# Optimization experiments

Measured on AMD Instinct MI355X. Metric: run time of the kernel, lower is better.

Reference implementation:

```python
import jax, jax.numpy as jnp
import numpy as np

NPOINT, RADIUS, NSAMPLE = 1024, 0.2, 32
EPS = 1e-5


def _fps(xyz, npoint):
    # Iterative farthest point sampling (deterministic start at index 0).
    B, N, _ = xyz.shape
    def step(carry, _):
        distance, farthest = carry
        centroid = jnp.take_along_axis(xyz, farthest[:, None, None], axis=1)  # (B,1,3)
        d = jnp.sum((xyz - centroid) ** 2, -1)                                # (B,N)
        distance = jnp.minimum(distance, d)
        return (distance, jnp.argmax(distance, -1)), farthest
    init = (jnp.full((B, N), 1e10, xyz.dtype), jnp.zeros((B,), jnp.int32))
    _, idx = jax.lax.scan(step, init, None, length=npoint)
    return idx.T  # (B, npoint)


def _gather(points, idx):
    # points (B,N,C), idx (B,S,K) -> (B,S,K,C)
    B, S, K = idx.shape
    flat = jnp.take_along_axis(points, idx.reshape(B, S * K)[:, :, None], axis=1)
    return flat.reshape(B, S, K, points.shape[-1])


def _query_ball(xyz, new_xyz):
    # For each centroid, first NSAMPLE point indices within RADIUS (pad with first hit).
    B, N, _ = xyz.shape
    sqr = jnp.sum((new_xyz[:, :, None, :] - xyz[:, None, :, :]) ** 2, -1)  # (B,S,N)
    gi = jnp.where(sqr > RADIUS ** 2, N, jnp.arange(N, dtype=jnp.int32)[None, None, :])
    gi = jnp.sort(gi, axis=-1)[:, :, :NSAMPLE]
    return jnp.where(gi == N, gi[:, :, :1], gi)  # (B,S,K)


def _cond_layer(x, t_embed, wt, bt, wc, bc, g, b):
    # ConditionalConv1d: x += time_mlp(gelu(t)); 1x1 conv; BatchNorm (batch stats); GELU.
    tp = jax.nn.gelu(t_embed, approximate=False) @ wt.T + bt      # (B,Cin)
    x = x + tp[:, None, None, :]
    y = jnp.einsum('bskc,oc->bsko', x, wc) + bc                   # (B,S,K,Cout)
    mu = jnp.mean(y, axis=(0, 1, 2))
    var = jnp.var(y, axis=(0, 1, 2))
    y = (y - mu) * jax.lax.rsqrt(var + EPS) * g + b
    return jax.nn.gelu(y, approximate=False)


def _forward(xyz, points, t_embed, params):
    fps_idx = _fps(xyz, NPOINT)                                        # (B,S)
    new_xyz = jnp.take_along_axis(xyz, fps_idx[:, :, None], axis=1)    # (B,S,3)
    idx = _query_ball(xyz, new_xyz)                                    # (B,S,K)
    grouped_xyz = _gather(xyz, idx) - new_xyz[:, :, None, :]           # (B,S,K,3)
    grouped_pts = _gather(jnp.swapaxes(points, 1, 2), idx)             # (B,S,K,C)
    x = jnp.concatenate([grouped_xyz, grouped_pts], -1)                # (B,S,K,C+3)
    for p in params:
        x = _cond_layer(x, t_embed, *p)
    new_points = jnp.swapaxes(jnp.max(x, axis=2), 1, 2)                # (B,Cout,S)
    return new_xyz, new_points


def setup_inputs() -> dict:
    key = jax.random.key(0)
    ks = iter(jax.random.split(key, 32))
    B, N, CIN, T = 8, 4096, 64, 128
    chans = [(CIN + 3, 64), (64, 64), (64, 128)]
    inp = {
        "xyz": jax.random.normal(next(ks), (B, N, 3), jnp.float32),
        "points": jax.random.normal(next(ks), (B, CIN, N), jnp.float32),
        "t_embed": jax.random.normal(next(ks), (B, T), jnp.float32),
    }
    for i, (ci, co) in enumerate(chans):
        inp[f"wt{i}"] = jax.random.normal(next(ks), (ci, T), jnp.float32) * 0.05
        inp[f"bt{i}"] = jnp.zeros((ci,), jnp.float32)
        inp[f"wc{i}"] = jax.random.normal(next(ks), (co, ci), jnp.float32) * 0.1
        inp[f"bc{i}"] = jnp.zeros((co,), jnp.float32)
        inp[f"g{i}"] = jnp.ones((co,), jnp.float32)
        inp[f"be{i}"] = jnp.zeros((co,), jnp.float32)
    return inp


def reference(xyz, points, t_embed,
              wt0, bt0, wc0, bc0, g0, be0,
              wt1, bt1, wc1, bc1, g1, be1,
              wt2, bt2, wc2, bc2, g2, be2):
    params = [(wt0, bt0, wc0, bc0, g0, be0),
              (wt1, bt1, wc1, bc1, g1, be1),
              (wt2, bt2, wc2, bc2, g2, be2)]
    return _forward(xyz, points, t_embed, params)
```

## Files before the change

kernel.cpp:

```cpp
#include <hip/hip_runtime.h>
#include <cmath>

#define Bc 8
#define Nc 4096
#define Sc 1024
#define Kc 32
#define Mc (Bc*Sc*Kc)

typedef float v2f __attribute__((ext_vector_type(2)));

__device__ __forceinline__ float gelu_f(float x){
  return 0.5f*x*(1.0f + erff(x*0.70710678f));
}

__device__ __forceinline__ v2f pk_add(v2f a, v2f b){
  v2f d; asm("v_pk_add_f32 %0, %1, %2" : "=v"(d) : "v"(a), "v"(b)); return d;
}
__device__ __forceinline__ v2f pk_mul(v2f a, v2f b){
  v2f d; asm("v_pk_mul_f32 %0, %1, %2" : "=v"(d) : "v"(a), "v"(b)); return d;
}

#define ROR_MAXF(v, n) { int _t = __builtin_amdgcn_update_dpp(__float_as_int(v), __float_as_int(v), 0x120|(n), 0xF, 0xF, false); \
                         v = fmaxf(v, __int_as_float(_t)); }
#define BC15_MAXF(v)   { int _t = __builtin_amdgcn_update_dpp(__float_as_int(v), __float_as_int(v), 0x142, 0xA, 0xF, false); \
                         v = fmaxf(v, __int_as_float(_t)); }
#define BC31_MAXF(v)   { int _t = __builtin_amdgcn_update_dpp(__float_as_int(v), __float_as_int(v), 0x143, 0xC, 0xF, false); \
                         v = fmaxf(v, __int_as_float(_t)); }

#define TK(v_, i_) { const bool _t = ((v_) > Bv) || (((v_) == Bv) && ((i_) < Bi)); \
  Bv = _t ? (v_) : Bv; Bi = _t ? (i_) : Bi; }

__global__ __launch_bounds__(256) void fused_front_kernel(
    const float* __restrict__ xyz, float* __restrict__ new_xyz,
    const float* __restrict__ points, float* __restrict__ pointsT,
    const float* __restrict__ t_embed,
    const float* __restrict__ wt0, const float* __restrict__ bt0,
    const float* __restrict__ wt1, const float* __restrict__ bt1,
    const float* __restrict__ wt2, const float* __restrict__ bt2,
    float* __restrict__ tp)
{
  __shared__ __align__(16) float smem[17424];
  const int bid = blockIdx.x;
  const int tid = threadIdx.x;

  if (bid < 8){
    const int b = bid;
    const int lane = tid & 63;
    const int wv = tid >> 6;
    const float* xb = xyz + b*Nc*3;
    float*    skv   = smem;
    unsigned* ski   = (unsigned*)(smem + 8);
    int*      shist = (int*)(smem + 16);
    float4*   c4    = (float4*)(smem + 1040);

    const int base = tid << 4;
    float4 f[12];
    const float4* src = (const float4*)(xb + base*3);
#pragma unroll
    for (int q=0;q<12;++q) f[q] = src[q];
#define AR(i) ((i)%4==0 ? f[(i)/4].x : (i)%4==1 ? f[(i)/4].y : (i)%4==2 ? f[(i)/4].z : f[(i)/4].w)
    v2f px2[8], py2[8], pz2[8], d2[8];
#pragma unroll
    for (int k=0;k<8;++k){
      px2[k].x = AR(6*k+0); py2[k].x = AR(6*k+1); pz2[k].x = AR(6*k+2);
      px2[k].y = AR(6*k+3); py2[k].y = AR(6*k+4); pz2[k].y = AR(6*k+5);
      c4[base+2*k  ] = make_float4(px2[k].x, py2[k].x, pz2[k].x, 0.f);
      c4[base+2*k+1] = make_float4(px2[k].y, py2[k].y, pz2[k].y, 0.f);
      d2[k].x = 1e10f; d2[k].y = 1e10f;
    }
#undef AR
    __syncthreads();
    int widx = 0;
    for (int it=0; it<Sc; ++it){
      const float4 cc = c4[widx];
      if (tid==0) shist[it] = widx;
      v2f ncx, ncy, ncz;
      ncx.x=-cc.x; ncx.y=-cc.x; ncy.x=-cc.y; ncy.y=-cc.y; ncz.x=-cc.z; ncz.y=-cc.z;
      float bvx=-1.0f, bvy=-1.0f;
#pragma unroll
      for (int k=0;k<8;++k){
        const v2f dx = pk_add(px2[k], ncx);
        const v2f dy = pk_add(py2[k], ncy);
        const v2f dz = pk_add(pz2[k], ncz);
        const v2f dd = pk_add(pk_add(pk_mul(dx,dx), pk_mul(dy,dy)), pk_mul(dz,dz));
        v2f dn;
        dn.x = fminf(d2[k].x, dd.x);
        dn.y = fminf(d2[k].y, dd.y);
        d2[k] = dn;
        bvx = fmaxf(bvx, dn.x);
        bvy = fmaxf(bvy, dn.y);
      }
      const float bv = fmaxf(bvx, bvy);
      unsigned bi_local = 0xFFFFFFFFu;
#pragma unroll
      for (int k=0;k<8;++k){
        const unsigned c0 = (d2[k].x == bv) ? (unsigned)(base + 2*k    ) : 0xFFFFFFFFu;
        const unsigned c1 = (d2[k].y == bv) ? (unsigned)(base + 2*k + 1) : 0xFFFFFFFFu;
        const unsigned cm = (c0 < c1) ? c0 : c1;
        bi_local = (cm < bi_local) ? cm : bi_local;
      }
      float mv = bv;
      ROR_MAXF(mv,1); ROR_MAXF(mv,2); ROR_MAXF(mv,4); ROR_MAXF(mv,8);
      BC15_MAXF(mv); BC31_MAXF(mv);
      mv = __int_as_float(__builtin_amdgcn_readlane(__float_as_int(mv), 63));
      const unsigned long long mk = __ballot(bv == mv);
      const int src_lane = __ffsll(mk) - 1;
      const unsigned bi = (unsigned)__builtin_amdgcn_readlane((int)bi_local, src_lane);
      const int p4 = (it & 1) << 2;
      if (lane==0){ skv[p4+wv] = mv; ski[p4+wv] = bi; }
      __syncthreads();
      const float4 m4 = *reinterpret_cast<const float4*>(&skv[p4]);
      const uint4  i4 = *reinterpret_cast<const uint4*>(&ski[p4]);
      float Bv = m4.x; unsigned Bi = i4.x;
      TK(m4.y, i4.y) TK(m4.z, i4.z) TK(m4.w, i4.w)
      widx = (int)Bi;
    }
    __syncthreads();
    for (int i = tid; i < Sc; i += 256){
      const float4 cc = c4[shist[i]];
      float* o = new_xyz + ((size_t)b*Sc + i)*3;
      o[0]=cc.x; o[1]=cc.y; o[2]=cc.z;
    }
  } else if (bid < 520){
    const int t  = bid - 8;
    const int tb = t >> 6;
    const int n0 = (t & 63) << 6;
    float (*tile)[65] = (float(*)[65])smem;
    const int sub = tid >> 6;
    const int ln  = tid & 63;
#pragma unroll 4
    for (int cp=0; cp<16; ++cp){
      const int c = (cp<<2) + sub;
      tile[c][ln] = points[((size_t)(tb*64+c))*Nc + n0 + ln];
    }
    __syncthreads();
#pragma unroll 4
    for (int np=0; np<16; ++np){
      const int nl = (np<<2) + sub;
      pointsT[((size_t)(tb*Nc + n0 + nl))*64 + ln] = tile[ln][nl];
    }
  } else {
    float* ge = smem;
    for (int i = tid; i < Bc*128; i += 256) ge[i] = gelu_f(t_embed[i]);
    __syncthreads();
    for (int i = tid; i < 3*Bc*68; i += 256){
      const int l = i / (Bc*68);
      const int r = i - l*(Bc*68);
      const int b = r / 68;
      const int c = r - b*68;
      const int ci = (l==0) ? 67 : 64;
      float v = 0.0f;
      if (c < ci){
        const float* wt = (l==0)?wt0:((l==1)?wt1:wt2);
        const float* bt = (l==0)?bt0:((l==1)?bt1:bt2);
        const float* w = wt + c*128;
        const float* g = ge + b*128;
        float acc = 0.0f;
        for (int t2=0;t2<128;++t2) acc = fmaf(g[t2], w[t2], acc);
        v = acc + bt[c];
      }
      tp[i] = v;
    }
  }
}

__global__ __launch_bounds__(256) void ballgather_kernel(const float* __restrict__ xyz,
    const float* __restrict__ new_xyz, const float* __restrict__ pointsT,
    float* __restrict__ X){
  const int g = (blockIdx.x<<2) + (threadIdx.x>>6);
  const int lane = threadIdx.x & 63;
  const int w = threadIdx.x >> 6;
  const int b = g >> 10;
  const float* xb = xyz + b*Nc*3;
  const float cx = new_xyz[g*3+0];
  const float cy = new_xyz[g*3+1];
  const float cz = new_xyz[g*3+2];
  __shared__ int sidx[4][32];
  int total = 0;
  for (int base=0; base<Nc; base+=64){
    const int i = base + lane;
    float dx=__fsub_rn(cx, xb[i*3+0]);
    float dy=__fsub_rn(cy, xb[i*3+1]);
    float dz=__fsub_rn(cz, xb[i*3+2]);
    float sq=__fadd_rn(__fadd_rn(__fmul_rn(dx,dx),__fmul_rn(dy,dy)),__fmul_rn(dz,dz));
    bool hit = !(sq > 0.04f);
    unsigned long long m = __ballot(hit);
    if (hit){
      int pos = total + (int)__popcll(m & ((1ull<<lane)-1ull));
      if (pos < 32) sidx[w][pos] = i;
    }
    total += (int)__popcll(m);
    if (total >= 32) break;
  }
  const int fill = (total < 32) ? total : 32;
  const int first = sidx[w][0];
  if (lane >= fill && lane < 32) sidx[w][lane] = first;
  for (int k=0; k<32; ++k){
    const int pidx = sidx[w][k];
    const float* pt = pointsT + ((size_t)((b<<12)+pidx))*64;
    float* xr = X + (size_t)((g<<5)+k)*68;
    float v;
    if      (lane==0) v = __fsub_rn(xb[pidx*3+0], cx);
    else if (lane==1) v = __fsub_rn(xb[pidx*3+1], cy);
    else if (lane==2) v = __fsub_rn(xb[pidx*3+2], cz);
    else              v = pt[lane-3];
    xr[lane] = v;
    if (lane < 4){
      const int c = 64 + lane;
      xr[c] = (c<67) ? pt[c-3] : 0.0f;
    }
  }
}

template<int NORMIN, int CI_REAL, int CI_PAD, int LDX>
__global__ __launch_bounds__(256) void mm_kernel(const float* X,
    const float* __restrict__ wc, const float* __restrict__ tp,
    const float* __restrict__ sc_in, const float* __restrict__ sh_in,
    float* Y, float* __restrict__ pS, float* __restrict__ pQ, int o_base)
{
  __shared__ __align__(16) float wT[CI_PAD][64];
  __shared__ __align__(16) float tpr[CI_PAD];
  __shared__ __align__(16) float scN[64], shN[64];
  __shared__ float redS[4][64];
  __shared__ float redQ[4][64];
  const int tid = threadIdx.x;
  const int m0 = blockIdx.x << 8;
  const int b  = blockIdx.x >> 7;
  for (int idx = tid; idx < CI_PAD*64; idx += 256){
    int c = idx >> 6, o = idx & 63;
    wT[c][o] = (c < CI_REAL) ? wc[(o_base + o)*CI_REAL + c] : 0.0f;
  }
  if (tid < CI_PAD) tpr[tid] = tp[b*68 + tid];
  if (NORMIN && tid < 64){ scN[tid] = sc_in[tid]; shN[tid] = sh_in[tid]; }
  __syncthreads();
  const int rg = tid >> 2, cg = tid & 3;
  const float* x0 = X + (size_t)(m0 + (rg<<2)) * LDX;
  float4 acc[4][4];
#pragma unroll
  for (int r=0;r<4;++r)
#pragma unroll
    for (int q=0;q<4;++q) acc[r][q] = make_float4(0.f,0.f,0.f,0.f);

  float4 xpf[4];
#pragma unroll
  for (int r=0;r<4;++r) xpf[r] = *reinterpret_cast<const float4*>(x0 + r*LDX);

#pragma unroll 1
  for (int c = 0; c < CI_PAD; c += 4){
    float4 xc[4];
#pragma unroll
    for (int r=0;r<4;++r) xc[r] = xpf[r];
    if (c + 4 < CI_PAD){
#pragma unroll
      for (int r=0;r<4;++r) xpf[r] = *reinterpret_cast<const float4*>(x0 + r*LDX + (c+4));
    }
    const float4 tpv = *reinterpret_cast<const float4*>(&tpr[c]);
    if (NORMIN){
      const float4 sci = *reinterpret_cast<const float4*>(&scN[c]);
      const float4 shi = *reinterpret_cast<const float4*>(&shN[c]);
#pragma unroll
      for (int r=0;r<4;++r){
        xc[r].x = gelu_f(fmaf(xc[r].x, sci.x, shi.x));
        xc[r].y = gelu_f(fmaf(xc[r].y, sci.y, shi.y));
        xc[r].z = gelu_f(fmaf(xc[r].z, sci.z, shi.z));
        xc[r].w = gelu_f(fmaf(xc[r].w, sci.w, shi.w));
      }
    }
    float4 xr[4];
#pragma unroll
    for (int r=0;r<4;++r)
      xr[r] = make_float4(xc[r].x+tpv.x, xc[r].y+tpv.y, xc[r].z+tpv.z, xc[r].w+tpv.w);
#pragma unroll
    for (int cc=0; cc<4; ++cc){
      const float* wrow = &wT[c+cc][cg<<4];
      const float4 w0 = *reinterpret_cast<const float4*>(wrow);
      const float4 w1 = *reinterpret_cast<const float4*>(wrow+4);
      const float4 w2 = *reinterpret_cast<const float4*>(wrow+8);
      const float4 w3 = *reinterpret_cast<const float4*>(wrow+12);
#pragma unroll
      for (int r=0;r<4;++r){
        const float xs = (cc==0)?xr[r].x:((cc==1)?xr[r].y:((cc==2)?xr[r].z:xr[r].w));
        acc[r][0].x = fmaf(xs, w0.x, acc[r][0].x);
        acc[r][0].y = fmaf(xs, w0.y, acc[r][0].y);
        acc[r][0].z = fmaf(xs, w0.z, acc[r][0].z);
        acc[r][0].w = fmaf(xs, w0.w, acc[r][0].w);
        acc[r][1].x = fmaf(xs, w1.x, acc[r][1].x);
        acc[r][1].y = fmaf(xs, w1.y, acc[r][1].y);
        acc[r][1].z = fmaf(xs, w1.z, acc[r][1].z);
        acc[r][1].w = fmaf(xs, w1.w, acc[r][1].w);
        acc[r][2].x = fmaf(xs, w2.x, acc[r][2].x);
        acc[r][2].y = fmaf(xs, w2.y, acc[r][2].y);
        acc[r][2].z = fmaf(xs, w2.z, acc[r][2].z);
        acc[r][2].w = fmaf(xs, w2.w, acc[r][2].w);
        acc[r][3].x = fmaf(xs, w3.x, acc[r][3].x);
        acc[r][3].y = fmaf(xs, w3.y, acc[r][3].y);
        acc[r][3].z = fmaf(xs, w3.z, acc[r][3].z);
        acc[r][3].w = fmaf(xs, w3.w, acc[r][3].w);
      }
    }
  }
#pragma unroll
  for (int r=0;r<4;++r){
    float4* yp = reinterpret_cast<float4*>(Y + (size_t)(m0 + (rg<<2) + r)*64 + (cg<<4));
#pragma unroll
    for (int q=0;q<4;++q) yp[q] = acc[r][q];
  }
  float4 s[4], q2[4];
#pragma unroll
  for (int q=0;q<4;++q){
    float sx=0,sy=0,sz=0,sw=0, qx=0,qy=0,qz=0,qw=0;
#pragma unroll
    for (int r=0;r<4;++r){
      sx+=acc[r][q].x; qx+=acc[r][q].x*acc[r][q].x;
      sy+=acc[r][q].y; qy+=acc[r][q].y*acc[r][q].y;
      sz+=acc[r][q].z; qz+=acc[r][q].z*acc[r][q].z;
      sw+=acc[r][q].w; qw+=acc[r][q].w*acc[r][q].w;
    }
    s[q]=make_float4(sx,sy,sz,sw); q2[q]=make_float4(qx,qy,qz,qw);
  }
  const int lane = tid & 63, wvv = tid >> 6;
#pragma unroll
  for (int off=32; off>=4; off>>=1){
#pragma unroll
    for (int q=0;q<4;++q){
      s[q].x  += __shfl_down(s[q].x,  off);
      s[q].y  += __shfl_down(s[q].y,  off);
      s[q].z  += __shfl_down(s[q].z,  off);
      s[q].w  += __shfl_down(s[q].w,  off);
      q2[q].x += __shfl_down(q2[q].x, off);
      q2[q].y += __shfl_down(q2[q].y, off);
      q2[q].z += __shfl_down(q2[q].z, off);
      q2[q].w += __shfl_down(q2[q].w, off);
    }
  }
  if (lane < 4){
#pragma unroll
    for (int q=0;q<4;++q){
      redS[wvv][lane*16 + q*4 + 0] = s[q].x;
      redS[wvv][lane*16 + q*4 + 1] = s[q].y;
      redS[wvv][lane*16 + q*4 + 2] = s[q].z;
      redS[wvv][lane*16 + q*4 + 3] = s[q].w;
      redQ[wvv][lane*16 + q*4 + 0] = q2[q].x;
      redQ[wvv][lane*16 + q*4 + 1] = q2[q].y;
      redQ[wvv][lane*16 + q*4 + 2] = q2[q].z;
      redQ[wvv][lane*16 + q*4 + 3] = q2[q].w;
    }
  }
  __syncthreads();
  if (tid < 64){
    float a=0.f, bb=0.f;
#pragma unroll
    for (int w2=0; w2<4; ++w2){ a += redS[w2][tid]; bb += redQ[w2][tid]; }
    pS[(blockIdx.x<<6) + tid] = a;
    pQ[(blockIdx.x<<6) + tid] = bb;
  }
}

__global__ __launch_bounds__(1024) void finalize_kernel(const float* __restrict__ pS,
    const float* __restrict__ pQ, const float* __restrict__ g, const float* __restrict__ be,
    float* __restrict__ scale, float* __restrict__ shift, int nblk){
  __shared__ float rS[16][64], rQ[16][64];
  const int o = threadIdx.x & 63;
  const int ch = threadIdx.x >> 6;
  const int per = nblk >> 4;
  float s=0.f, q=0.f;
  const int i0 = ch*per;
#pragma unroll 4
  for (int i=0;i<per;++i){
    s += pS[((i0+i)<<6)+o];
    q += pQ[((i0+i)<<6)+o];
  }
  rS[ch][o]=s; rQ[ch][o]=q;
  __syncthreads();
  if (threadIdx.x < 64){
    float ss = 0.f, qq = 0.f;
#pragma unroll
    for (int c=0;c<16;++c){ ss += rS[c][o]; qq += rQ[c][o]; }
    const float inv_n = 1.0f/(float)Mc;
    const float mu = ss*inv_n;
    const float var = qq*inv_n - mu*mu;
    const float rs = 1.0f/sqrtf(var + 1e-5f);
    const float sc = rs*g[o];
    scale[o] = sc;
    shift[o] = fmaf(-mu, sc, be[o]);
  }
}

__global__ __launch_bounds__(256) void pool_kernel(const float* __restrict__ Y,
    const float* __restrict__ scale, const float* __restrict__ shift,
    float* __restrict__ out, int o_base){
  __shared__ float pool[32][65];
  const int tid = threadIdx.x;
  const int b  = blockIdx.x >> 5;
  const int s0 = (blockIdx.x & 31) << 5;
  const int c  = tid & 63;
  const int sl0 = tid >> 6;
  const float sc = scale[c], sh = shift[c];
  for (int sp=0; sp<8; ++sp){
    const int sl = (sp<<2) + sl0;
    const int s = s0 + sl;
    const float* yp = Y + ((size_t)((b<<10)+s)<<5)*64 + c;
    float mx = -1e30f;
#pragma unroll 4
    for (int k=0;k<32;++k){
      float v = yp[(size_t)(k<<6)];
      v = gelu_f(fmaf(v, sc, sh));
      mx = fmaxf(mx, v);
    }
    pool[sl][c] = mx;
  }
  __syncthreads();
  for (int p=0;p<8;++p){
    const int c2 = (p<<3) + (tid>>5);
    const int sl = tid & 31;
    out[((size_t)((b<<7) + o_base + c2)<<10) + s0 + sl] = pool[sl][c2];
  }
}

extern "C" void kernel_launch(void* const* d_in, const int* in_sizes, int n_in,
                              void* d_out, int out_size, void* d_ws, size_t ws_size,
                              hipStream_t stream){
  const float* xyz     = (const float*)d_in[0];
  const float* points  = (const float*)d_in[1];
  const float* t_embed = (const float*)d_in[2];
  const float* wt0=(const float*)d_in[3],  *bt0=(const float*)d_in[4],  *wc0=(const float*)d_in[5];
  const float* g0 =(const float*)d_in[7],  *be0=(const float*)d_in[8];
  const float* wt1=(const float*)d_in[9],  *bt1=(const float*)d_in[10], *wc1=(const float*)d_in[11];
  const float* g1 =(const float*)d_in[13], *be1=(const float*)d_in[14];
  const float* wt2=(const float*)d_in[15], *bt2=(const float*)d_in[16], *wc2=(const float*)d_in[17];
  const float* g2 =(const float*)d_in[19], *be2=(const float*)d_in[20];

  float* out_xyz = (float*)d_out;
  float* out_pts = (float*)d_out + Bc*Sc*3;

  float* ws       = (float*)d_ws;
  float* tp       = ws + 0;
  float* pointsT  = ws + 2048;
  float* pS1      = ws + 2099200;
  float* pQ1      = ws + 2230272;
  float* X        = ws + 2361344;
  float* Ya       = ws + 20187136;
  float* pS0      = ws + 36964352;
  float* pQ0      = ws + 37095424;
  float* sc0      = ws + 37226496;
  float* sh0      = sc0 + 64;
  float* sc1      = sc0 + 128;
  float* sh1      = sc0 + 192;
  float* sc2      = sc0 + 256;
  float* sh2      = sc0 + 320;
  float* sc3      = sc0 + 384;
  float* sh3      = sc0 + 448;
  float* Yx       = X;

  const int NBLK = Mc/256;

  fused_front_kernel<<<521, 256, 0, stream>>>(xyz, out_xyz, points, pointsT,
      t_embed, wt0,bt0, wt1,bt1, wt2,bt2, tp);
  ballgather_kernel<<<(Bc*Sc)/4, 256, 0, stream>>>(xyz, out_xyz, pointsT, X);

  mm_kernel<0,67,68,68><<<NBLK, 256, 0, stream>>>(X, wc0, tp, nullptr, nullptr, Ya, pS0, pQ0, 0);
  finalize_kernel<<<1, 1024, 0, stream>>>(pS0, pQ0, g0, be0, sc0, sh0, NBLK);

  mm_kernel<1,64,64,64><<<NBLK, 256, 0, stream>>>(Ya, wc1, tp + 544, sc0, sh0, Ya, pS0, pQ0, 0);
  finalize_kernel<<<1, 1024, 0, stream>>>(pS0, pQ0, g1, be1, sc1, sh1, NBLK);

  mm_kernel<1,64,64,64><<<NBLK, 256, 0, stream>>>(Ya, wc2, tp + 1088, sc1, sh1, Yx, pS0, pQ0, 0);
  mm_kernel<1,64,64,64><<<NBLK, 256, 0, stream>>>(Ya, wc2, tp + 1088, sc1, sh1, Ya, pS1, pQ1, 64);
  finalize_kernel<<<1, 1024, 0, stream>>>(pS0, pQ0, g2,    be2,    sc2, sh2, NBLK);
  finalize_kernel<<<1, 1024, 0, stream>>>(pS1, pQ1, g2+64, be2+64, sc3, sh3, NBLK);

  pool_kernel<<<Bc*Sc/32, 256, 0, stream>>>(Yx, sc2, sh2, out_pts, 0);
  pool_kernel<<<Bc*Sc/32, 256, 0, stream>>>(Ya, sc3, sh3, out_pts, 64);
}
```

Before: 1.211 ms.

## Fuse the two half-width layer-3 matmul passes into one 128-output kernel

Adds mm2_kernel, which computes all 128 output channels of the last conditional layer in one pass. Each row's input is read once, and the BatchNorm-GELU on it is applied once; before, two launches each did this for a 64-channel half. The per-channel statistics for all 128 outputs are merged into a single templated finalize launch, and the workspace partial buffers are re-laid out to fit the wider partials. The cost is a larger register tile per thread (64 float accumulators), which may lower occupancy. It also keeps in-place writes into Ya, which rely on lanes that share rows sitting in the same wavefront.

```diff
diff --git a/kernel.cpp b/kernel.cpp
--- a/kernel.cpp
+++ b/kernel.cpp
@@ -356,26 +356,140 @@
   }
 }
 
+__global__ __launch_bounds__(256) void mm2_kernel(const float* X,
+    const float* __restrict__ wc, const float* __restrict__ tp,
+    const float* __restrict__ sc_in, const float* __restrict__ sh_in,
+    float* Y0, float* Y1, float* __restrict__ pS, float* __restrict__ pQ)
+{
+  __shared__ __align__(16) float wT[64][128];
+  __shared__ __align__(16) float tpr[64];
+  __shared__ __align__(16) float scN[64], shN[64];
+  __shared__ float redS[4][128];
+  __shared__ float redQ[4][128];
+  const int tid = threadIdx.x;
+  const int m0 = blockIdx.x << 7;
+  const int b  = blockIdx.x >> 8;
+  for (int idx = tid; idx < 64*128; idx += 256){
+    const int c = idx >> 7, o = idx & 127;
+    wT[c][o] = wc[o*64 + c];
+  }
+  if (tid < 64) tpr[tid] = tp[b*68 + tid];
+  else if (tid < 128) scN[tid-64] = sc_in[tid-64];
+  else if (tid < 192) shN[tid-128] = sh_in[tid-128];
+  __syncthreads();
+  const int rg = tid >> 2, cg = tid & 3;
+  const int cb = cg << 2;
+  const float* x0 = X + (size_t)(m0 + (rg<<1)) * 64;
+  float4 acc[2][8];
+#pragma unroll
+  for (int r=0;r<2;++r)
+#pragma unroll
+    for (int q=0;q<8;++q) acc[r][q] = make_float4(0.f,0.f,0.f,0.f);
+
+  float4 xpf[2];
+  xpf[0] = *reinterpret_cast<const float4*>(x0);
+  xpf[1] = *reinterpret_cast<const float4*>(x0 + 64);
+
+#pragma unroll 1
+  for (int c = 0; c < 64; c += 4){
+    float4 xc[2]; xc[0]=xpf[0]; xc[1]=xpf[1];
+    if (c + 4 < 64){
+      xpf[0] = *reinterpret_cast<const float4*>(x0 + (c+4));
+      xpf[1] = *reinterpret_cast<const float4*>(x0 + 64 + (c+4));
+    }
+    const float4 tpv = *reinterpret_cast<const float4*>(&tpr[c]);
+    const float4 sci = *reinterpret_cast<const float4*>(&scN[c]);
+    const float4 shi = *reinterpret_cast<const float4*>(&shN[c]);
+#pragma unroll
+    for (int r=0;r<2;++r){
+      xc[r].x = gelu_f(fmaf(xc[r].x, sci.x, shi.x)) + tpv.x;
+      xc[r].y = gelu_f(fmaf(xc[r].y, sci.y, shi.y)) + tpv.y;
+      xc[r].z = gelu_f(fmaf(xc[r].z, sci.z, shi.z)) + tpv.z;
+      xc[r].w = gelu_f(fmaf(xc[r].w, sci.w, shi.w)) + tpv.w;
+    }
+#pragma unroll
+    for (int cc=0; cc<4; ++cc){
+      const float xs0 = (cc==0)?xc[0].x:((cc==1)?xc[0].y:((cc==2)?xc[0].z:xc[0].w));
+      const float xs1 = (cc==0)?xc[1].x:((cc==1)?xc[1].y:((cc==2)?xc[1].z:xc[1].w));
+      const float* wrow = &wT[c+cc][cb];
+#pragma unroll
+      for (int j=0;j<8;++j){
+        const float4 wv = *reinterpret_cast<const float4*>(wrow + (j<<4));
+        acc[0][j].x = fmaf(xs0, wv.x, acc[0][j].x);
+        acc[0][j].y = fmaf(xs0, wv.y, acc[0][j].y);
+        acc[0][j].z = fmaf(xs0, wv.z, acc[0][j].z);
+        acc[0][j].w = fmaf(xs0, wv.w, acc[0][j].w);
+        acc[1][j].x = fmaf(xs1, wv.x, acc[1][j].x);
+        acc[1][j].y = fmaf(xs1, wv.y, acc[1][j].y);
+        acc[1][j].z = fmaf(xs1, wv.z, acc[1][j].z);
+        acc[1][j].w = fmaf(xs1, wv.w, acc[1][j].w);
+      }
+    }
+  }
+#pragma unroll
+  for (int r=0;r<2;++r){
+    const size_t row = (size_t)(m0 + (rg<<1) + r);
+#pragma unroll
+    for (int j=0;j<8;++j){
+      float* yb = (j<4) ? Y0 : Y1;
+      const int col = ((j<4) ? (j<<4) : ((j-4)<<4)) + cb;
+      *reinterpret_cast<float4*>(yb + row*64 + col) = acc[r][j];
+    }
+  }
+  const int lane = tid & 63, wvv = tid >> 6;
+#pragma unroll
+  for (int j=0;j<8;++j){
+    float4 s = make_float4(acc[0][j].x+acc[1][j].x, acc[0][j].y+acc[1][j].y,
+                           acc[0][j].z+acc[1][j].z, acc[0][j].w+acc[1][j].w);
+    float4 q2 = make_float4(acc[0][j].x*acc[0][j].x + acc[1][j].x*acc[1][j].x,
+                            acc[0][j].y*acc[0][j].y + acc[1][j].y*acc[1][j].y,
+                            acc[0][j].z*acc[0][j].z + acc[1][j].z*acc[1][j].z,
+                            acc[0][j].w*acc[0][j].w + acc[1][j].w*acc[1][j].w);
+#pragma unroll
+    for (int off=32; off>=4; off>>=1){
+      s.x += __shfl_down(s.x, off);   s.y += __shfl_down(s.y, off);
+      s.z += __shfl_down(s.z, off);   s.w += __shfl_down(s.w, off);
+      q2.x += __shfl_down(q2.x, off); q2.y += __shfl_down(q2.y, off);
+      q2.z += __shfl_down(q2.z, off); q2.w += __shfl_down(q2.w, off);
+    }
+    if (lane < 4){
+      const int ch = (j<<4) + (lane<<2);
+      redS[wvv][ch+0]=s.x;  redS[wvv][ch+1]=s.y;  redS[wvv][ch+2]=s.z;  redS[wvv][ch+3]=s.w;
+      redQ[wvv][ch+0]=q2.x; redQ[wvv][ch+1]=q2.y; redQ[wvv][ch+2]=q2.z; redQ[wvv][ch+3]=q2.w;
+    }
+  }
+  __syncthreads();
+  if (tid < 128){
+    float a=0.f, bb=0.f;
+#pragma unroll
+    for (int w2=0; w2<4; ++w2){ a += redS[w2][tid]; bb += redQ[w2][tid]; }
+    pS[(size_t)blockIdx.x*128 + tid] = a;
+    pQ[(size_t)blockIdx.x*128 + tid] = bb;
+  }
+}
+
+template<int CO>
 __global__ __launch_bounds__(1024) void finalize_kernel(const float* __restrict__ pS,
     const float* __restrict__ pQ, const float* __restrict__ g, const float* __restrict__ be,
     float* __restrict__ scale, float* __restrict__ shift, int nblk){
-  __shared__ float rS[16][64], rQ[16][64];
-  const int o = threadIdx.x & 63;
-  const int ch = threadIdx.x >> 6;
-  const int per = nblk >> 4;
+  __shared__ float rS[1024], rQ[1024];
+  constexpr int NCH = 1024 / CO;
+  const int o  = threadIdx.x & (CO-1);
+  const int ch = threadIdx.x / CO;
+  const int per = nblk / NCH;
+  const int i0 = ch * per;
   float s=0.f, q=0.f;
-  const int i0 = ch*per;
 #pragma unroll 4
   for (int i=0;i<per;++i){
-    s += pS[((i0+i)<<6)+o];
-    q += pQ[((i0+i)<<6)+o];
-  }
-  rS[ch][o]=s; rQ[ch][o]=q;
+    s += pS[(size_t)(i0+i)*CO + o];
+    q += pQ[(size_t)(i0+i)*CO + o];
+  }
+  rS[threadIdx.x]=s; rQ[threadIdx.x]=q;
   __syncthreads();
-  if (threadIdx.x < 64){
+  if (threadIdx.x < CO){
     float ss = 0.f, qq = 0.f;
 #pragma unroll
-    for (int c=0;c<16;++c){ ss += rS[c][o]; qq += rQ[c][o]; }
+    for (int c=0;c<NCH;++c){ ss += rS[c*CO+o]; qq += rQ[c*CO+o]; }
     const float inv_n = 1.0f/(float)Mc;
     const float mu = ss*inv_n;
     const float var = qq*inv_n - mu*mu;
@@ -436,20 +550,16 @@
   float* ws       = (float*)d_ws;
   float* tp       = ws + 0;
   float* pointsT  = ws + 2048;
-  float* pS1      = ws + 2099200;
-  float* pQ1      = ws + 2230272;
+  float* pS       = ws + 2099200;
   float* X        = ws + 2361344;
   float* Ya       = ws + 20187136;
-  float* pS0      = ws + 36964352;
-  float* pQ0      = ws + 37095424;
+  float* pQ       = ws + 36964352;
   float* sc0      = ws + 37226496;
   float* sh0      = sc0 + 64;
   float* sc1      = sc0 + 128;
   float* sh1      = sc0 + 192;
   float* sc2      = sc0 + 256;
-  float* sh2      = sc0 + 320;
-  float* sc3      = sc0 + 384;
-  float* sh3      = sc0 + 448;
+  float* sh2      = sc0 + 384;
   float* Yx       = X;
 
   const int NBLK = Mc/256;
@@ -458,17 +568,15 @@
       t_embed, wt0,bt0, wt1,bt1, wt2,bt2, tp);
   ballgather_kernel<<<(Bc*Sc)/4, 256, 0, stream>>>(xyz, out_xyz, pointsT, X);
 
-  mm_kernel<0,67,68,68><<<NBLK, 256, 0, stream>>>(X, wc0, tp, nullptr, nullptr, Ya, pS0, pQ0, 0);
-  finalize_kernel<<<1, 1024, 0, stream>>>(pS0, pQ0, g0, be0, sc0, sh0, NBLK);
-
-  mm_kernel<1,64,64,64><<<NBLK, 256, 0, stream>>>(Ya, wc1, tp + 544, sc0, sh0, Ya, pS0, pQ0, 0);
-  finalize_kernel<<<1, 1024, 0, stream>>>(pS0, pQ0, g1, be1, sc1, sh1, NBLK);
-
-  mm_kernel<1,64,64,64><<<NBLK, 256, 0, stream>>>(Ya, wc2, tp + 1088, sc1, sh1, Yx, pS0, pQ0, 0);
-  mm_kernel<1,64,64,64><<<NBLK, 256, 0, stream>>>(Ya, wc2, tp + 1088, sc1, sh1, Ya, pS1, pQ1, 64);
-  finalize_kernel<<<1, 1024, 0, stream>>>(pS0, pQ0, g2,    be2,    sc2, sh2, NBLK);
-  finalize_kernel<<<1, 1024, 0, stream>>>(pS1, pQ1, g2+64, be2+64, sc3, sh3, NBLK);
-
-  pool_kernel<<<Bc*Sc/32, 256, 0, stream>>>(Yx, sc2, sh2, out_pts, 0);
-  pool_kernel<<<Bc*Sc/32, 256, 0, stream>>>(Ya, sc3, sh3, out_pts, 64);
-}
+  mm_kernel<0,67,68,68><<<NBLK, 256, 0, stream>>>(X, wc0, tp, nullptr, nullptr, Ya, pS, pQ, 0);
+  finalize_kernel<64><<<1, 1024, 0, stream>>>(pS, pQ, g0, be0, sc0, sh0, NBLK);
+
+  mm_kernel<1,64,64,64><<<NBLK, 256, 0, stream>>>(Ya, wc1, tp + 544, sc0, sh0, Ya, pS, pQ, 0);
+  finalize_kernel<64><<<1, 1024, 0, stream>>>(pS, pQ, g1, be1, sc1, sh1, NBLK);
+
+  mm2_kernel<<<Mc/128, 256, 0, stream>>>(Ya, wc2, tp + 1088, sc1, sh1, Yx, Ya, pS, pQ);
+  finalize_kernel<128><<<1, 1024, 0, stream>>>(pS, pQ, g2, be2, sc2, sh2, Mc/128);
+
+  pool_kernel<<<Bc*Sc/32, 256, 0, stream>>>(Yx, sc2,    sh2,    out_pts, 0);
+  pool_kernel<<<Bc*Sc/32, 256, 0, stream>>>(Ya, sc2+64, sh2+64, out_pts, 64);
+}
```

Measured after the change: 1.176 ms, median of 2. -2.9%, faster.
